# Kernel tuning notes

Hardware: AMD Instinct MI355X
Metric: run time of the kernel (lower is better)

Reference implementation:

```python
import jax, jax.numpy as jnp
import numpy as np

B, N, M = 8, 4096, 4096


def setup_inputs() -> dict:
    key = jax.random.key(0)
    ks = jax.random.split(key, 8)
    return {
        "x_aligned": jax.random.normal(ks[0], (B, N, 3), dtype=jnp.float32),
        "y": jax.random.normal(ks[1], (B, M, 3), dtype=jnp.float32),
        "R": jax.random.normal(ks[2], (B, 3, 3), dtype=jnp.float32),
        "S": jax.random.normal(ks[3], (B, 3), dtype=jnp.float32),
        "t": jax.random.normal(ks[4], (B, 3, 1), dtype=jnp.float32),
        "R_gt": jax.random.normal(ks[5], (B, 3, 3), dtype=jnp.float32),
        "S_gt": jax.random.normal(ks[6], (B, 3), dtype=jnp.float32),
        "t_gt": jax.random.normal(ks[7], (B, 3), dtype=jnp.float32),
    }


def chamfer_distance(x, y):
    # x: [B,N,3], y: [B,M,3]; bidirectional mean squared NN distance
    xn = jnp.sum(x * x, axis=-1)                      # [B,N]
    yn = jnp.sum(y * y, axis=-1)                      # [B,M]
    xy = jnp.einsum('bnd,bmd->bnm', x, y)             # [B,N,M]
    d2 = xn[:, :, None] + yn[:, None, :] - 2.0 * xy   # [B,N,M] squared dists
    cham_x = jnp.mean(jnp.min(d2, axis=2), axis=1)    # [B] x -> y
    cham_y = jnp.mean(jnp.min(d2, axis=1), axis=1)    # [B] y -> x
    return jnp.mean(cham_x) + jnp.mean(cham_y)        # batch mean, summed dirs


def reference(x_aligned, y, R, S, t, R_gt, S_gt, t_gt):
    t = jnp.squeeze(t)                                # [B,3]
    eye = jnp.eye(3, dtype=R.dtype)
    R_loss = jnp.einsum('bij,bkj->bik', R, R_gt) - eye  # R @ R_gt^T - I
    L_reg = (jnp.sum(R_loss * R_loss)
             + jnp.sum((S - S_gt) ** 2)
             + jnp.sum((t - t_gt) ** 2))
    L_chamfer = chamfer_distance(x_aligned, y)
    return L_reg + L_chamfer
```

## Files before the change

### kernel.cpp

```cpp
#include <hip/hip_runtime.h>

#define BB 8
#define NN 4096
#define MC 256
#define NCHUNK (NN / MC)
#define KPT 4
#define TPB 256
#define PTS_PER_BLOCK (TPB * KPT)
#define NPTS (2 * BB * NN)


__global__ __launch_bounds__(TPB) void chamfer_partial(
    const float* __restrict__ X, const float* __restrict__ Y,
    float* __restrict__ partial, float* __restrict__ out) {
  __shared__ float4 ly[MC];
  const int tid = threadIdx.x;
  const int zb  = blockIdx.z;
  const int b   = zb & (BB - 1);
  const int dir = zb >> 3;
  const float* pts  = dir ? (Y + b * NN * 3) : (X + b * NN * 3);
  const float* refs = dir ? (X + b * NN * 3) : (Y + b * NN * 3);
  const int c = blockIdx.y;

  if (tid == 0 && blockIdx.x == 0 && blockIdx.y == 0 && blockIdx.z == 0)
    *out = 0.0f;

  {
    const int j = c * MC + tid;
    const float a0 = refs[j * 3 + 0];
    const float a1 = refs[j * 3 + 1];
    const float a2 = refs[j * 3 + 2];
    ly[tid] = make_float4(-2.0f * a0, -2.0f * a1, -2.0f * a2,
                          a0 * a0 + a1 * a1 + a2 * a2);
  }
  __syncthreads();

  float px[KPT], py[KPT], pz[KPT], m[KPT];
  const int p0 = blockIdx.x * PTS_PER_BLOCK + tid;
#pragma unroll
  for (int k = 0; k < KPT; k++) {
    const int p = p0 + k * TPB;
    px[k] = pts[p * 3 + 0];
    py[k] = pts[p * 3 + 1];
    pz[k] = pts[p * 3 + 2];
    m[k] = 1e30f;
  }

#define CHAMFER_BODY(w0, w1, w2, w3)                                           \
  _Pragma("unroll") for (int k = 0; k < KPT; k++) {                            \
    const float s0 =                                                           \
        fmaf(px[k], w0.x, fmaf(py[k], w0.y, fmaf(pz[k], w0.z, w0.w)));         \
    const float s1 =                                                           \
        fmaf(px[k], w1.x, fmaf(py[k], w1.y, fmaf(pz[k], w1.z, w1.w)));         \
    const float s2 =                                                           \
        fmaf(px[k], w2.x, fmaf(py[k], w2.y, fmaf(pz[k], w2.z, w2.w)));         \
    const float s3 =                                                           \
        fmaf(px[k], w3.x, fmaf(py[k], w3.y, fmaf(pz[k], w3.z, w3.w)));         \
    m[k] = fminf(m[k], fminf(fminf(s0, s1), fminf(s2, s3)));                   \
  }

  float4 w0 = ly[0], w1 = ly[1], w2 = ly[2], w3 = ly[3];
#pragma unroll 2
  for (int j = 0; j < MC - 4; j += 4) {
    const float4 n0 = ly[j + 4];
    const float4 n1 = ly[j + 5];
    const float4 n2 = ly[j + 6];
    const float4 n3 = ly[j + 7];
    CHAMFER_BODY(w0, w1, w2, w3)
    w0 = n0; w1 = n1; w2 = n2; w3 = n3;
  }
  CHAMFER_BODY(w0, w1, w2, w3)
#undef CHAMFER_BODY

#pragma unroll
  for (int k = 0; k < KPT; k++) {
    const int p = p0 + k * TPB;
    const float pn = px[k] * px[k] + py[k] * py[k] + pz[k] * pz[k];
    partial[(c * (2 * BB) + zb) * NN + p] = m[k] + pn;
  }
}

__global__ __launch_bounds__(256) void chamfer_reduce(
    const float4* __restrict__ partial4,
    const float* __restrict__ R, const float* __restrict__ S,
    const float* __restrict__ t, const float* __restrict__ Rgt,
    const float* __restrict__ Sgt, const float* __restrict__ tgt,
    float* __restrict__ out) {
  const int tid = threadIdx.x;
  const int q4 = blockIdx.x * 256 + tid;
  float4 mn = make_float4(1e30f, 1e30f, 1e30f, 1e30f);
#pragma unroll
  for (int c = 0; c < NCHUNK; c++) {
    const float4 v = partial4[c * (NPTS / 4) + q4];
    mn.x = fminf(mn.x, v.x);
    mn.y = fminf(mn.y, v.y);
    mn.z = fminf(mn.z, v.z);
    mn.w = fminf(mn.w, v.w);
  }
  float s = (mn.x + mn.y) + (mn.z + mn.w);
  for (int o = 32; o > 0; o >>= 1) s += __shfl_down(s, o);
  __shared__ float wsum[4];
  if ((tid & 63) == 0) wsum[tid >> 6] = s;
  __syncthreads();
  if (tid == 0) {
    const float bs = wsum[0] + wsum[1] + wsum[2] + wsum[3];
    atomicAdd(out, bs * (1.0f / (float)(BB * NN)));
  }

  if (blockIdx.x == 0) {
    float v = 0.0f;
    if (tid < 72) {
      const int b = tid / 9, ik = tid % 9, i = ik / 3, k = ik % 3;
      const float* Rb = R + b * 9;
      const float* Gb = Rgt + b * 9;
      float d = Rb[i * 3 + 0] * Gb[k * 3 + 0] +
                Rb[i * 3 + 1] * Gb[k * 3 + 1] +
                Rb[i * 3 + 2] * Gb[k * 3 + 2];
      d -= (i == k) ? 1.0f : 0.0f;
      v = d * d;
    } else if (tid < 96) {
      const int i = tid - 72;
      const float d = S[i] - Sgt[i];
      v = d * d;
    } else if (tid < 120) {
      const int i = tid - 96;
      const float d = t[i] - tgt[i];
      v = d * d;
    }
    for (int o = 32; o > 0; o >>= 1) v += __shfl_down(v, o);
    __shared__ float rsum[4];
    if ((tid & 63) == 0) rsum[tid >> 6] = v;
    __syncthreads();
    if (tid == 0) atomicAdd(out, rsum[0] + rsum[1] + rsum[2] + rsum[3]);
  }
}

extern "C" void kernel_launch(void* const* d_in, const int* in_sizes, int n_in,
                              void* d_out, int out_size, void* d_ws, size_t ws_size,
                              hipStream_t stream) {
  const float* X   = (const float*)d_in[0];
  const float* Y   = (const float*)d_in[1];
  const float* R   = (const float*)d_in[2];
  const float* S   = (const float*)d_in[3];
  const float* t   = (const float*)d_in[4];
  const float* Rgt = (const float*)d_in[5];
  const float* Sgt = (const float*)d_in[6];
  const float* tgt = (const float*)d_in[7];

  float* partial = (float*)d_ws;
  float* out     = (float*)d_out;

  dim3 gA(NN / PTS_PER_BLOCK, NCHUNK, 2 * BB);
  chamfer_partial<<<gA, TPB, 0, stream>>>(X, Y, partial, out);

  chamfer_reduce<<<NPTS / 4 / 256, 256, 0, stream>>>(
      (const float4*)partial, R, S, t, Rgt, Sgt, tgt, out);
}
```

Measured before the change: 91.06 us.

## Compute chamfer distance dot products with split-bf16 MFMA instead of scalar FMA

Adds a prep kernel that splits coordinates and norms into three bf16 terms each (hi, mid, lo) and packs them into MFMA-ready A and B layouts. The main kernel then evaluates the -2x·y + |y|^2 term with 16x16x32 bf16 MFMA instructions, taking a running min over the accumulator outputs, followed by a cross-lane min reduction. This moves the O(N·M) pairwise work from vector FMAs onto the matrix cores, using bf16x3 splitting to stay close to fp32 accuracy. The cost is an extra launch, a workspace round-trip for the packed data, and a small precision difference from the dropped low-order cross terms.

After: 102.6 us. 12.7% more time.

```diff
diff --git a/kernel.cpp b/kernel.cpp
--- a/kernel.cpp
+++ b/kernel.cpp
@@ -2,82 +2,142 @@
 
 #define BB 8
 #define NN 4096
+#define NZB 16
 #define MC 256
 #define NCHUNK (NN / MC)
-#define KPT 4
 #define TPB 256
-#define PTS_PER_BLOCK (TPB * KPT)
-#define NPTS (2 * BB * NN)
-
-
-__global__ __launch_bounds__(TPB) void chamfer_partial(
+#define NPTS (NZB * NN)
+
+typedef short short8 __attribute__((ext_vector_type(8)));
+typedef float f32x4 __attribute__((ext_vector_type(4)));
+
+#define APACK_SHORTS (NZB * NCHUNK * 8192)
+#define BPACK_SHORTS (NZB * NN * 32)
+
+__device__ __forceinline__ unsigned short b16(float v) {
+  const unsigned u = __float_as_uint(v);
+  return (unsigned short)((u + 0x7fffu + ((u >> 16) & 1u)) >> 16);
+}
+__device__ __forceinline__ float fb16(unsigned short h) {
+  return __uint_as_float(((unsigned)h) << 16);
+}
+__device__ __forceinline__ void split3(float v, unsigned short* o) {
+  const unsigned short h0 = b16(v); const float f0 = fb16(h0);
+  const unsigned short h1 = b16(v - f0); const float f1 = fb16(h1);
+  const unsigned short h2 = b16(v - f0 - f1);
+  o[0] = h0; o[1] = h1; o[2] = h2;
+}
+
+__global__ __launch_bounds__(TPB) void hegn_prep(
     const float* __restrict__ X, const float* __restrict__ Y,
-    float* __restrict__ partial, float* __restrict__ out) {
-  __shared__ float4 ly[MC];
+    unsigned short* __restrict__ Apack, unsigned short* __restrict__ Bpack,
+    float* __restrict__ qn, float* __restrict__ out) {
+  const int id = blockIdx.x * TPB + threadIdx.x;
+  if (id == 0) *out = 0.0f;
+  const int role = id >> 16;
+  const int zb = (id >> 12) & 15;
+  const int j = id & (NN - 1);
+  const int b = zb & 7;
+  const int dir = zb >> 3;
+  const float* src = (role == 0) ? (dir ? X + b * NN * 3 : Y + b * NN * 3)
+                                 : (dir ? Y + b * NN * 3 : X + b * NN * 3);
+  const float a0 = src[j * 3 + 0];
+  const float a1 = src[j * 3 + 1];
+  const float a2 = src[j * 3 + 2];
+  unsigned short s0[3], s1[3], s2[3];
+  if (role == 0) {
+    split3(a0, s0); split3(a1, s1); split3(a2, s2);
+    const float n = fmaf(a0, a0, fmaf(a1, a1, a2 * a2));
+    unsigned short n3[3]; split3(n, n3);
+    unsigned short* dst = Apack + (zb * NCHUNK + (j >> 8)) * 8192 +
+                          (((j >> 4) & 15) * 64 + (j & 15)) * 8;
+    const unsigned short* r[3] = {s0, s1, s2};
+#pragma unroll
+    for (int d = 0; d < 3; d++) {
+      short8 w;
+      w[0] = r[d][0]; w[1] = r[d][0]; w[2] = r[d][1]; w[3] = r[d][1];
+      w[4] = r[d][0]; w[5] = r[d][2]; w[6] = r[d][1]; w[7] = r[d][2];
+      *(short8*)(dst + d * 128) = w;
+    }
+    short8 w;
+    w[0] = n3[0]; w[1] = n3[1]; w[2] = n3[2];
+    w[3] = 0; w[4] = 0; w[5] = 0; w[6] = 0; w[7] = 0;
+    *(short8*)(dst + 3 * 128) = w;
+  } else {
+    split3(-2.0f * a0, s0); split3(-2.0f * a1, s1); split3(-2.0f * a2, s2);
+    unsigned short* dst = Bpack + (zb * NN + j) * 32;
+    const unsigned short* s[3] = {s0, s1, s2};
+#pragma unroll
+    for (int d = 0; d < 3; d++) {
+      short8 w;
+      w[0] = s[d][0]; w[1] = s[d][1]; w[2] = s[d][0]; w[3] = s[d][1];
+      w[4] = s[d][2]; w[5] = s[d][0]; w[6] = s[d][2]; w[7] = s[d][1];
+      *(short8*)(dst + d * 8) = w;
+    }
+    short8 w;
+    w[0] = (short)0x3f80; w[1] = (short)0x3f80; w[2] = (short)0x3f80;
+    w[3] = 0; w[4] = 0; w[5] = 0; w[6] = 0; w[7] = 0;
+    *(short8*)(dst + 24) = w;
+    qn[zb * NN + j] = fmaf(a0, a0, fmaf(a1, a1, a2 * a2));
+  }
+}
+
+__global__ __launch_bounds__(TPB) void hegn_chamfer(
+    const unsigned short* __restrict__ Apack,
+    const unsigned short* __restrict__ Bpack,
+    const float* __restrict__ qn, float* __restrict__ partial) {
+  __shared__ short8 As[1024];
   const int tid = threadIdx.x;
-  const int zb  = blockIdx.z;
-  const int b   = zb & (BB - 1);
-  const int dir = zb >> 3;
-  const float* pts  = dir ? (Y + b * NN * 3) : (X + b * NN * 3);
-  const float* refs = dir ? (X + b * NN * 3) : (Y + b * NN * 3);
-  const int c = blockIdx.y;
-
-  if (tid == 0 && blockIdx.x == 0 && blockIdx.y == 0 && blockIdx.z == 0)
-    *out = 0.0f;
+  const int zb = blockIdx.z;
+  const int c  = blockIdx.y;
+  const int l  = tid & 63;
+  const int wid = tid >> 6;
+  const int wavebase = blockIdx.x * 512 + wid * 128;
 
   {
-    const int j = c * MC + tid;
-    const float a0 = refs[j * 3 + 0];
-    const float a1 = refs[j * 3 + 1];
-    const float a2 = refs[j * 3 + 2];
-    ly[tid] = make_float4(-2.0f * a0, -2.0f * a1, -2.0f * a2,
-                          a0 * a0 + a1 * a1 + a2 * a2);
-  }
+    const float4* src = (const float4*)(Apack + (zb * NCHUNK + c) * 8192);
+    float4* dst = (float4*)As;
+#pragma unroll
+    for (int i = 0; i < 4; i++) dst[i * TPB + tid] = src[i * TPB + tid];
+  }
+
+  const int col = l & 15, kb = l >> 4;
+  short8 Bf[8]; float qf[8];
+#pragma unroll
+  for (int f = 0; f < 8; f++) {
+    const int q = wavebase + f * 16 + col;
+    Bf[f] = *(const short8*)(Bpack + (zb * NN + q) * 32 + kb * 8);
+    qf[f] = qn[zb * NN + q];
+  }
+  float m[8];
+#pragma unroll
+  for (int f = 0; f < 8; f++) m[f] = 1e30f;
+  const f32x4 Z = {0.0f, 0.0f, 0.0f, 0.0f};
   __syncthreads();
 
-  float px[KPT], py[KPT], pz[KPT], m[KPT];
-  const int p0 = blockIdx.x * PTS_PER_BLOCK + tid;
-#pragma unroll
-  for (int k = 0; k < KPT; k++) {
-    const int p = p0 + k * TPB;
-    px[k] = pts[p * 3 + 0];
-    py[k] = pts[p * 3 + 1];
-    pz[k] = pts[p * 3 + 2];
-    m[k] = 1e30f;
-  }
-
-#define CHAMFER_BODY(w0, w1, w2, w3)                                           \
-  _Pragma("unroll") for (int k = 0; k < KPT; k++) {                            \
-    const float s0 =                                                           \
-        fmaf(px[k], w0.x, fmaf(py[k], w0.y, fmaf(pz[k], w0.z, w0.w)));         \
-    const float s1 =                                                           \
-        fmaf(px[k], w1.x, fmaf(py[k], w1.y, fmaf(pz[k], w1.z, w1.w)));         \
-    const float s2 =                                                           \
-        fmaf(px[k], w2.x, fmaf(py[k], w2.y, fmaf(pz[k], w2.z, w2.w)));         \
-    const float s3 =                                                           \
-        fmaf(px[k], w3.x, fmaf(py[k], w3.y, fmaf(pz[k], w3.z, w3.w)));         \
-    m[k] = fminf(m[k], fminf(fminf(s0, s1), fminf(s2, s3)));                   \
-  }
-
-  float4 w0 = ly[0], w1 = ly[1], w2 = ly[2], w3 = ly[3];
 #pragma unroll 2
-  for (int j = 0; j < MC - 4; j += 4) {
-    const float4 n0 = ly[j + 4];
-    const float4 n1 = ly[j + 5];
-    const float4 n2 = ly[j + 6];
-    const float4 n3 = ly[j + 7];
-    CHAMFER_BODY(w0, w1, w2, w3)
-    w0 = n0; w1 = n1; w2 = n2; w3 = n3;
-  }
-  CHAMFER_BODY(w0, w1, w2, w3)
-#undef CHAMFER_BODY
-
-#pragma unroll
-  for (int k = 0; k < KPT; k++) {
-    const int p = p0 + k * TPB;
-    const float pn = px[k] * px[k] + py[k] * py[k] + pz[k] * pz[k];
-    partial[(c * (2 * BB) + zb) * NN + p] = m[k] + pn;
-  }
+  for (int tt = 0; tt < 16; tt++) {
+    const short8 A = As[tt * 64 + l];
+#pragma unroll
+    for (int f = 0; f < 8; f++) {
+      const f32x4 D = __builtin_amdgcn_mfma_f32_16x16x32_bf16(A, Bf[f], Z, 0, 0, 0);
+      m[f] = fminf(m[f], fminf(fminf(D[0], D[1]), fminf(D[2], D[3])));
+    }
+  }
+
+#pragma unroll
+  for (int f = 0; f < 8; f++) {
+    float v = m[f];
+    v = fminf(v, __shfl_xor(v, 16));
+    v = fminf(v, __shfl_xor(v, 32));
+    m[f] = v + qf[f];
+  }
+  const int g = l >> 4;
+  const float v1 = g == 0 ? m[0] : g == 1 ? m[1] : g == 2 ? m[2] : m[3];
+  const float v2 = g == 0 ? m[4] : g == 1 ? m[5] : g == 2 ? m[6] : m[7];
+  float* pp = partial + (c * NZB + zb) * NN + wavebase;
+  pp[l] = v1;
+  pp[64 + l] = v2;
 }
 
 __global__ __launch_bounds__(256) void chamfer_reduce(
@@ -147,11 +207,16 @@
   const float* Sgt = (const float*)d_in[6];
   const float* tgt = (const float*)d_in[7];
 
-  float* partial = (float*)d_ws;
-  float* out     = (float*)d_out;
-
-  dim3 gA(NN / PTS_PER_BLOCK, NCHUNK, 2 * BB);
-  chamfer_partial<<<gA, TPB, 0, stream>>>(X, Y, partial, out);
+  unsigned short* Apack = (unsigned short*)d_ws;
+  unsigned short* Bpack = Apack + APACK_SHORTS;
+  float* qn       = (float*)(Bpack + BPACK_SHORTS);
+  float* partial  = qn + NPTS;
+  float* out      = (float*)d_out;
+
+  hegn_prep<<<2 * NZB * NN / TPB, TPB, 0, stream>>>(X, Y, Apack, Bpack, qn, out);
+
+  dim3 gC(8, NCHUNK, NZB);
+  hegn_chamfer<<<gC, TPB, 0, stream>>>(Apack, Bpack, qn, partial);
 
   chamfer_reduce<<<NPTS / 4 / 256, 256, 0, stream>>>(
       (const float4*)partial, R, S, t, Rgt, Sgt, tgt, out);
```
